# Kernel tuning notes

Measured on AMD Instinct MI355X. Metric: run time of the kernel, lower is better.

Reference implementation:

```python
import jax, jax.numpy as jnp
import numpy as np

# FFM: 20 fields x 500 features each, k=16
NUM_FIELDS = 20
FIELD_SIZE = 500
TOTAL_FEATURES = NUM_FIELDS * FIELD_SIZE  # 10000
K = 16
BATCH = 4096


def setup_inputs() -> dict:
    key = jax.random.key(0)
    kx, kw, kv = jax.random.split(key, 3)
    x = jax.random.uniform(kx, (BATCH, TOTAL_FEATURES), dtype=jnp.float32)
    w = jax.random.normal(kw, (TOTAL_FEATURES, 1), dtype=jnp.float32)
    v = jax.random.normal(kv, (NUM_FIELDS, TOTAL_FEATURES, K), dtype=jnp.float32)
    return {"x": x, "w": w, "v": v}


def reference(x, w, v):
    B = x.shape[0]
    F, S, k = NUM_FIELDS, FIELD_SIZE, K
    # linear term: [B, 1]
    linear = x @ w
    # group features by field (fields are contiguous, equal-sized)
    xr = x.reshape(B, F, S)            # [b, field i, feat within field]
    vr = v.reshape(F, F, S, k)         # [field g (other), field i, feat, k]
    # E[b, g, i, :] = sum over features of field i of x * v[g]
    # i.e. field-i embedding specialized for interaction with field g
    E = jnp.einsum('bis,gisk->bgik', xr, vr)  # [B, F, F, K]
    # pairwise term: sum_{i<j} <E[b, j, i], E[b, i, j]>
    T = jnp.einsum('bjik,bijk->bij', E, E)    # [B, F, F]
    mask = jnp.triu(jnp.ones((F, F), dtype=bool), 1)
    pair = jnp.sum(jnp.where(mask, T, 0.0), axis=(1, 2))[:, None]  # [B, 1]
    return linear + pair
```

## Files before the change

kernel.cpp:

```cpp
#include <hip/hip_runtime.h>
#include <stdint.h>


#define NF 20
#define FS 500
#define TFEAT 10000
#define KD 16
#define NCOL 336
#define NFRG 21
#define KP 512
#define NB 4096
#define ROWE (NF * NCOL)

typedef __bf16 bf16x8 __attribute__((ext_vector_type(8)));
typedef __bf16 bf16x2 __attribute__((ext_vector_type(2)));
typedef float  f32x4  __attribute__((ext_vector_type(4)));
typedef unsigned int u32x4 __attribute__((ext_vector_type(4)));

typedef __attribute__((address_space(1))) const void* as1cv;
typedef __attribute__((address_space(3))) void* as3v;

__device__ inline void gload_lds16(const void* g, void* l) {
  __builtin_amdgcn_global_load_lds((as1cv)g, (as3v)l, 16, 0, 0);
}

__global__ __launch_bounds__(256) void prep_vt(const float* __restrict__ v,
                                               const float* __restrict__ w,
                                               __bf16* __restrict__ VtS) {
  const int i = blockIdx.x / NFRG;
  const int q = blockIdx.x % NFRG;
  const int tdx = threadIdx.x;
  __shared__ float lv[FS * 17];
  if (q < NF) {
    const int k = tdx & 15, sb = tdx >> 4;
    const float* vb = v + ((size_t)q * TFEAT + (size_t)i * FS) * KD;
    for (int it = 0; it < 32; ++it) {
      int s = it * 16 + sb;
      if (s < FS) lv[s * 17 + k] = vb[(size_t)s * KD + k];
    }
    __syncthreads();
  }
  const float* wf = w + (size_t)i * FS;
  __bf16* base = VtS + ((size_t)i * 16 * NFRG + q) * 512;
  for (int it = 0; it < 4; ++it) {
    int p = it * 256 + tdx;
    int t = p >> 6, l = p & 63;
    int r = l >> 2;
    int kk = t * 32 + (((l & 3) ^ ((l >> 3) & 3)) << 3);
    bf16x8 h;
#pragma unroll
    for (int e = 0; e < 8; ++e) {
      int s = kk + e;
      float val = 0.f;
      if (s < FS) {
        if (q < NF) val = lv[s * 17 + r];
        else if (r == 0) val = wf[s];
      }
      h[e] = (__bf16)val;
    }
    *(bf16x8*)(base + (size_t)t * (NFRG * 512) + l * 8) = h;
  }
}

__global__ __launch_bounds__(256, 3) void k1_gemm(
    const float* __restrict__ x, const __bf16* __restrict__ VtS,
    __bf16* __restrict__ E2, int chunk_base, int tiles) {
  __shared__ __bf16 As[2][64][32];
  __shared__ __bf16 Bs[2][NCOL * 32];

  int bid = blockIdx.x;
  const int nwg = gridDim.x;
  if ((nwg & 7) == 0) {
    int cpx = nwg >> 3;
    bid = (bid & 7) * cpx + (bid >> 3);
  }
  const int i  = bid / tiles;
  const int tb = bid % tiles;
  const int tid = threadIdx.x;
  const int lane = tid & 63, wid = tid >> 6;
  const int b0 = chunk_base + tb * 64;

  const int arow = tid >> 2;
  const int ac16 = (tid & 3) * 16;
  const int ah  = (tid & 3) >> 1;
  const int gh0 = (2 * (tid & 3)) & 3;
  const int rsw = (arow >> 1) & 3;
  const float* xrow = x + (size_t)(b0 + arow) * TFEAT + i * FS;
  const __bf16* VtSi = VtS + (size_t)i * 16 * NFRG * 512 + lane * 8;

  auto issueB = [&](int t) {
#pragma unroll
    for (int jj = 0; jj < 6; ++jj) {
      int q = wid + 4 * jj;
      if (q < NFRG) {
        gload_lds16(VtSi + ((size_t)(2 * t) * NFRG + q) * 512,
                    (void*)&Bs[0][q * 512]);
        gload_lds16(VtSi + ((size_t)(2 * t + 1) * NFRG + q) * 512,
                    (void*)&Bs[1][q * 512]);
      }
    }
  };

  f32x4 ar_[4];
  auto aload = [&](int t) {
#pragma unroll
    for (int j = 0; j < 4; ++j) {
      int c = t * 64 + ac16 + j * 4;
      if (c > 496) c = 496;
      ar_[j] = *(const f32x4*)(xrow + c);
    }
  };
  auto astore = [&]() {
    bf16x8 h0, h1;
#pragma unroll
    for (int e = 0; e < 4; ++e) {
      h0[e] = (__bf16)ar_[0][e]; h0[4 + e] = (__bf16)ar_[1][e];
      h1[e] = (__bf16)ar_[2][e]; h1[4 + e] = (__bf16)ar_[3][e];
    }
    *(bf16x8*)(&As[ah][arow][((gh0)     ^ rsw) * 8]) = h0;
    *(bf16x8*)(&As[ah][arow][((gh0 + 1) ^ rsw) * 8]) = h1;
  };

  const int nfr = wid ? 5 : 6;
  const int Fbase = wid ? (1 + wid * 5) : 0;
  const int ar = lane & 15, akc = lane >> 4;

  f32x4 acc[4][6];
#pragma unroll
  for (int m = 0; m < 4; ++m)
#pragma unroll
    for (int nf = 0; nf < 6; ++nf) acc[m][nf] = (f32x4){0.f, 0.f, 0.f, 0.f};

  aload(0);
  issueB(0);
  astore();
  asm volatile("s_waitcnt vmcnt(0) lgkmcnt(0)" ::: "memory");
  __builtin_amdgcn_s_barrier();

  for (int t = 0; t < 8; ++t) {
    if (t < 7) aload(t + 1);
    __builtin_amdgcn_sched_barrier(0);

#pragma unroll
    for (int ks = 0; ks < 2; ++ks) {
      bf16x8 af[4];
#pragma unroll
      for (int m = 0; m < 4; ++m) {
        int row = m * 16 + ar;
        int pch = akc ^ ((row >> 1) & 3);
        af[m] = *(const bf16x8*)(&As[ks][row][pch * 8]);
      }
#pragma unroll
      for (int nf = 0; nf < 6; ++nf)
        if (nf < nfr) {
          int n_ = (Fbase + nf) * 16 + ar;
          int pc = akc ^ ((n_ >> 1) & 3);
          bf16x8 bfr = *(const bf16x8*)&Bs[ks][n_ * 32 + pc * 8];
#pragma unroll
          for (int m = 0; m < 4; ++m)
            acc[m][nf] = __builtin_amdgcn_mfma_f32_16x16x32_bf16(af[m], bfr,
                                                                 acc[m][nf], 0, 0, 0);
        }
    }
    if (t < 7) {
      __builtin_amdgcn_s_barrier();
      issueB(t + 1);
      astore();
      asm volatile("s_waitcnt vmcnt(0) lgkmcnt(0)" ::: "memory");
      __builtin_amdgcn_s_barrier();
    }
  }

  const int lr4 = akc * 4, lcol = lane & 15;
#pragma unroll
  for (int m = 0; m < 4; ++m)
#pragma unroll
    for (int nf = 0; nf < 6; ++nf)
      if (nf < nfr) {
        int n = (Fbase + nf) * 16 + lcol;
#pragma unroll
        for (int r = 0; r < 4; ++r) {
          int bl = tb * 64 + m * 16 + lr4 + r;
          E2[(size_t)bl * ROWE + i * NCOL + n] = (__bf16)acc[m][nf][r];
        }
      }
}

__global__ __launch_bounds__(256) void k2_pair(
    const __bf16* __restrict__ E2, float* __restrict__ out, int chunk_base) {
  __shared__ __align__(16) unsigned shw[4][3360];
  const int tid = threadIdx.x, lane = tid & 63, wid = tid >> 6;
  const int bl = blockIdx.x * 4 + wid;
  const unsigned* src = (const unsigned*)(E2 + (size_t)bl * ROWE);
  for (int it = 0; it < 14; ++it) {
    int idx = it * 64 + lane;
    if (idx < 840) {
      u32x4 val = *(const u32x4*)(src + (size_t)idx * 4);
      *(u32x4*)&shw[wid][idx * 4] = val;
    }
  }
  __syncthreads();
  const __bf16* sh = (const __bf16*)shw[wid];
  const int k = lane & 15, g = lane >> 4;
  float sum = 0.f;
  for (int i = g; i < NF; i += 4)
    for (int j = i + 1; j < NF; ++j)
      sum += (float)sh[i * NCOL + j * 16 + k] * (float)sh[j * NCOL + i * 16 + k];
  if (lane < NF) sum += (float)sh[lane * NCOL + 320];
#pragma unroll
  for (int off = 32; off; off >>= 1) sum += __shfl_xor(sum, off);
  if (lane == 0) out[chunk_base + bl] = sum;
}

extern "C" void kernel_launch(void* const* d_in, const int* in_sizes, int n_in,
                              void* d_out, int out_size, void* d_ws, size_t ws_size,
                              hipStream_t stream) {
  const float* x = (const float*)d_in[0];
  const float* w = (const float*)d_in[1];
  const float* v = (const float*)d_in[2];
  float* out = (float*)d_out;
  char* ws = (char*)d_ws;

  const size_t vt_bytes = (size_t)NF * 16 * NFRG * 512 * 2;
  __bf16* VtS = (__bf16*)ws;
  __bf16* E2 = (__bf16*)(ws + vt_bytes);

  size_t eavail = (ws_size > vt_bytes) ? ws_size - vt_bytes : 0;
  int Bc = NB;
  while (Bc > 64 && (size_t)Bc * ROWE * 2 > eavail) Bc >>= 1;

  prep_vt<<<NF * NFRG, 256, 0, stream>>>(v, w, VtS);
  for (int cb = 0; cb < NB; cb += Bc) {
    int tiles = Bc / 64;
    k1_gemm<<<NF * tiles, 256, 0, stream>>>(x, VtS, E2, cb, tiles);
    k2_pair<<<Bc / 4, 256, 0, stream>>>(E2, out, cb);
  }
}
```

Baseline: 72.60 us.

## Split GEMM K-step into halves to overlap B/A staging with MFMA compute

The k1_gemm main loop now stages the B tile and the bf16 A tile per 32-wide half instead of per 64-wide step. The load for one half is issued while MFMAs run on the other half, and a partial vmcnt wait lets the prefetched x registers stay in flight. This is meant to hide global-to-LDS latency that was previously exposed behind a full barrier each step. Wave priority is also raised around the MFMA section with s_setprio. The cost is an extra barrier per step and more delicate waitcnt bookkeeping.

```diff
diff --git a/kernel.cpp b/kernel.cpp
--- a/kernel.cpp
+++ b/kernel.cpp
@@ -88,16 +88,13 @@
   const float* xrow = x + (size_t)(b0 + arow) * TFEAT + i * FS;
   const __bf16* VtSi = VtS + (size_t)i * 16 * NFRG * 512 + lane * 8;
 
-  auto issueB = [&](int t) {
+  auto issueBhalf = [&](int t32) {
+    __bf16* dst = &Bs[t32 & 1][0];
 #pragma unroll
     for (int jj = 0; jj < 6; ++jj) {
       int q = wid + 4 * jj;
-      if (q < NFRG) {
-        gload_lds16(VtSi + ((size_t)(2 * t) * NFRG + q) * 512,
-                    (void*)&Bs[0][q * 512]);
-        gload_lds16(VtSi + ((size_t)(2 * t + 1) * NFRG + q) * 512,
-                    (void*)&Bs[1][q * 512]);
-      }
+      if (q < NFRG)
+        gload_lds16(VtSi + ((size_t)t32 * NFRG + q) * 512, (void*)(dst + q * 512));
     }
   };
 
@@ -110,15 +107,17 @@
       ar_[j] = *(const f32x4*)(xrow + c);
     }
   };
-  auto astore = [&]() {
-    bf16x8 h0, h1;
-#pragma unroll
-    for (int e = 0; e < 4; ++e) {
-      h0[e] = (__bf16)ar_[0][e]; h0[4 + e] = (__bf16)ar_[1][e];
-      h1[e] = (__bf16)ar_[2][e]; h1[4 + e] = (__bf16)ar_[3][e];
-    }
-    *(bf16x8*)(&As[ah][arow][((gh0)     ^ rsw) * 8]) = h0;
-    *(bf16x8*)(&As[ah][arow][((gh0 + 1) ^ rsw) * 8]) = h1;
+  auto astoreH = [&](int half) {
+    if (ah == half) {
+      bf16x8 h0, h1;
+#pragma unroll
+      for (int e = 0; e < 4; ++e) {
+        h0[e] = (__bf16)ar_[0][e]; h0[4 + e] = (__bf16)ar_[1][e];
+        h1[e] = (__bf16)ar_[2][e]; h1[4 + e] = (__bf16)ar_[3][e];
+      }
+      *(bf16x8*)(&As[ah][arow][((gh0)     ^ rsw) * 8]) = h0;
+      *(bf16x8*)(&As[ah][arow][((gh0 + 1) ^ rsw) * 8]) = h1;
+    }
   };
 
   const int nfr = wid ? 5 : 6;
@@ -131,41 +130,56 @@
 #pragma unroll
     for (int nf = 0; nf < 6; ++nf) acc[m][nf] = (f32x4){0.f, 0.f, 0.f, 0.f};
 
+  auto compute = [&](int h) {
+    __builtin_amdgcn_s_setprio(1);
+    bf16x8 af[4];
+#pragma unroll
+    for (int m = 0; m < 4; ++m) {
+      int row = m * 16 + ar;
+      int pch = akc ^ ((row >> 1) & 3);
+      af[m] = *(const bf16x8*)(&As[h][row][pch * 8]);
+    }
+#pragma unroll
+    for (int nf = 0; nf < 6; ++nf)
+      if (nf < nfr) {
+        int n_ = (Fbase + nf) * 16 + ar;
+        int pc = akc ^ ((n_ >> 1) & 3);
+        bf16x8 bfr = *(const bf16x8*)&Bs[h][n_ * 32 + pc * 8];
+#pragma unroll
+        for (int m = 0; m < 4; ++m)
+          acc[m][nf] = __builtin_amdgcn_mfma_f32_16x16x32_bf16(af[m], bfr,
+                                                               acc[m][nf], 0, 0, 0);
+      }
+    __builtin_amdgcn_s_setprio(0);
+  };
+
   aload(0);
-  issueB(0);
-  astore();
+  issueBhalf(0);
+  astoreH(0);
   asm volatile("s_waitcnt vmcnt(0) lgkmcnt(0)" ::: "memory");
   __builtin_amdgcn_s_barrier();
 
   for (int t = 0; t < 8; ++t) {
+    issueBhalf(2 * t + 1);
+    __builtin_amdgcn_sched_barrier(0);
+    astoreH(1);
     if (t < 7) aload(t + 1);
     __builtin_amdgcn_sched_barrier(0);
-
-#pragma unroll
-    for (int ks = 0; ks < 2; ++ks) {
-      bf16x8 af[4];
-#pragma unroll
-      for (int m = 0; m < 4; ++m) {
-        int row = m * 16 + ar;
-        int pch = akc ^ ((row >> 1) & 3);
-        af[m] = *(const bf16x8*)(&As[ks][row][pch * 8]);
-      }
-#pragma unroll
-      for (int nf = 0; nf < 6; ++nf)
-        if (nf < nfr) {
-          int n_ = (Fbase + nf) * 16 + ar;
-          int pc = akc ^ ((n_ >> 1) & 3);
-          bf16x8 bfr = *(const bf16x8*)&Bs[ks][n_ * 32 + pc * 8];
-#pragma unroll
-          for (int m = 0; m < 4; ++m)
-            acc[m][nf] = __builtin_amdgcn_mfma_f32_16x16x32_bf16(af[m], bfr,
-                                                                 acc[m][nf], 0, 0, 0);
-        }
-    }
+    compute(0);
+    if (t < 7)
+      asm volatile("s_waitcnt vmcnt(4) lgkmcnt(0)" ::: "memory");
+    else
+      asm volatile("s_waitcnt vmcnt(0) lgkmcnt(0)" ::: "memory");
+    __builtin_amdgcn_s_barrier();
+
     if (t < 7) {
-      __builtin_amdgcn_s_barrier();
-      issueB(t + 1);
-      astore();
+      issueBhalf(2 * t + 2);
+      __builtin_amdgcn_sched_barrier(0);
+      astoreH(0);
+    }
+    __builtin_amdgcn_sched_barrier(0);
+    compute(1);
+    if (t < 7) {
       asm volatile("s_waitcnt vmcnt(0) lgkmcnt(0)" ::: "memory");
       __builtin_amdgcn_s_barrier();
     }
```

After: 77.33 us. 1.07x slower.
